# Optimization experiments

Measured on AMD Instinct MI355X. Metric: run time of the kernel, lower is better.

## Reference

```python
import jax, jax.numpy as jnp
import numpy as np

STATE_DIM = 128
NUM_STATES = 16
BATCH = 16384


def setup_inputs() -> dict:
    key = jax.random.key(0)
    k1, k2, k3, k4 = jax.random.split(key, 4)
    x = jax.random.normal(k1, (BATCH, STATE_DIM), dtype=jnp.float32)
    state_idx = jax.random.randint(k2, (BATCH,), 0, NUM_STATES)
    A_all = jax.random.normal(k3, (NUM_STATES, STATE_DIM, STATE_DIM), dtype=jnp.float32)
    C_all = jax.random.normal(k4, (NUM_STATES, STATE_DIM, STATE_DIM), dtype=jnp.float32)
    return {"x": x, "state_idx": state_idx, "A_all": A_all, "C_all": C_all}


def reference(x, state_idx, A_all, C_all):
    # Per-sample expert matrix gather: [B, D, D]
    Ag = A_all[state_idx]
    Cg = C_all[state_idx]
    # state = relu(x @ A_i) per sample, batched via einsum
    state = jax.nn.relu(jnp.einsum('bd,bde->be', x, Ag))
    # observation = state @ C_i
    out = jnp.einsum('be,bef->bf', state, Cg)
    return out
```

## Files before the change

kernel.cpp:

```cpp
#include <hip/hip_runtime.h>

#define D 128
#define NS 16
#define BATCH 16384
#define TILE 32
#define NTB 32

typedef __attribute__((ext_vector_type(8))) short short8;
typedef __attribute__((ext_vector_type(4))) float f32x4;

__device__ __forceinline__ unsigned short f2bf(float f) {
  unsigned u = __builtin_bit_cast(unsigned, f);
  u += 0x7FFFu + ((u >> 16) & 1u);
  return (unsigned short)(u >> 16);
}

#define CPAD 32

__global__ __launch_bounds__(256) void prep_kernel(
    const float* __restrict__ A_all, const float* __restrict__ C_all,
    const int* __restrict__ sidx,
    int* __restrict__ counts, unsigned short* __restrict__ lists,
    unsigned short* __restrict__ At, unsigned short* __restrict__ Ct) {
  const int b = blockIdx.x, tid = threadIdx.x;
  if (b < 128) {
    __shared__ float T[32][129];
    const int mat = b >> 6, r = b & 63, s = r >> 2, slab = r & 3;
    const float* in = (mat ? C_all : A_all) + (size_t)s * D * D;
    unsigned short* outp = (mat ? Ct : At) + (size_t)s * D * D;
    const int e0 = slab * 32;
    const int ecol = (tid & 7) * 4;
    const int drow = tid >> 3;
#pragma unroll
    for (int i = 0; i < 4; i++) {
      const int d = drow + 32 * i;
      const float4 v = *(const float4*)(in + (size_t)d * D + e0 + ecol);
      T[ecol + 0][d] = v.x;
      T[ecol + 1][d] = v.y;
      T[ecol + 2][d] = v.z;
      T[ecol + 3][d] = v.w;
    }
    __syncthreads();
    const int e = tid >> 3;
    const int d0 = (tid & 7) * 16;
    unsigned short p[16];
#pragma unroll
    for (int k = 0; k < 16; k++) p[k] = f2bf(T[e][d0 + k]);
    unsigned short* dst = outp + (size_t)(e0 + e) * D + d0;
    *(uint4*)(dst) = *(const uint4*)(p);
    *(uint4*)(dst + 8) = *(const uint4*)(p + 8);
  } else {
    __shared__ int wcnt[4][NS];
    __shared__ int woff[4][NS];
    __shared__ int sbase[NS];
    const int i = (b - 128) * 256 + tid;
    const int s = sidx[i];
    const int lane = tid & 63, w = tid >> 6;
    int myrank = 0;
#pragma unroll 1
    for (int ss = 0; ss < NS; ss++) {
      unsigned long long m = __ballot(s == ss);
      if (s == ss) myrank = (int)__popcll(m & ((1ull << lane) - 1ull));
      if (lane == 0) wcnt[w][ss] = (int)__popcll(m);
    }
    __syncthreads();
    if (tid < NS) {
      const int c0 = wcnt[0][tid], c1 = wcnt[1][tid];
      const int c2 = wcnt[2][tid], c3 = wcnt[3][tid];
      sbase[tid] = atomicAdd(&counts[tid * CPAD], c0 + c1 + c2 + c3);
      woff[0][tid] = 0;
      woff[1][tid] = c0;
      woff[2][tid] = c0 + c1;
      woff[3][tid] = c0 + c1 + c2;
    }
    __syncthreads();
    lists[(size_t)s * BATCH + sbase[s] + woff[w][s] + myrank] = (unsigned short)i;
  }
}

__global__ __launch_bounds__(256, 3) void ssm_kernel(
    const float* __restrict__ x,
    const int* __restrict__ counts,
    const unsigned short* __restrict__ lists,
    const unsigned short* __restrict__ At,
    const unsigned short* __restrict__ Ct,
    float* __restrict__ out) {
  __shared__ unsigned short Xs[TILE][136];
  __shared__ unsigned short Hs[TILE][136];
  __shared__ unsigned short Ws[D][136];
  __shared__ int rows[TILE];

  const int s = blockIdx.y;
  const int n = counts[s * CPAD];
  const int tid = threadIdx.x;
  const int lane = tid & 63, w = tid >> 6;
  const int l15 = lane & 15, quad = lane >> 4;
  const int wr = w & 1, wc = w >> 1;

  for (int t0 = blockIdx.x; t0 * TILE < n; t0 += NTB) {
    if (t0 != blockIdx.x) __syncthreads();
    const int row0 = t0 * TILE;
    const int nr = min(TILE, n - row0);
    const size_t lb = (size_t)s * BATCH + row0;

    uint4 ctr[8];
    {
      const uint4* g = (const uint4*)(Ct + (size_t)s * D * D);
#pragma unroll
      for (int i = 0; i < 8; i++) ctr[i] = g[i * 256 + tid];
    }

    {
      const int r = tid >> 3, q = tid & 7;
      int rid = (r < nr) ? (int)lists[lb + r] : -1;
      if (q == 0) rows[r] = rid;
      unsigned short* xr = &Xs[r][q * 16];
      if (rid >= 0) {
        const float4* src = (const float4*)(x + (size_t)rid * D + q * 16);
#pragma unroll
        for (int i = 0; i < 4; i++) {
          float4 v = src[i];
          ushort4 p;
          p.x = f2bf(v.x); p.y = f2bf(v.y); p.z = f2bf(v.z); p.w = f2bf(v.w);
          *(ushort4*)(xr + i * 4) = p;
        }
      } else {
        ushort4 z; z.x = z.y = z.z = z.w = 0;
#pragma unroll
        for (int i = 0; i < 4; i++) *(ushort4*)(xr + i * 4) = z;
      }
    }
    {
      const uint4* g = (const uint4*)(At + (size_t)s * D * D);
#pragma unroll
      for (int i = 0; i < 8; i++) {
        const int c = i * 256 + tid;
        *(uint4*)&Ws[c >> 4][(c & 15) * 8] = g[c];
      }
    }
    __syncthreads();

    f32x4 acc[4];
#pragma unroll
    for (int nb = 0; nb < 4; nb++) acc[nb] = (f32x4){0.f, 0.f, 0.f, 0.f};
#pragma unroll
    for (int kb = 0; kb < 4; kb++) {
      short8 aF = *(const short8*)&Xs[wr * 16 + l15][kb * 32 + quad * 8];
#pragma unroll
      for (int nb = 0; nb < 4; nb++) {
        short8 bF = *(const short8*)&Ws[wc * 64 + nb * 16 + l15][kb * 32 + quad * 8];
        acc[nb] = __builtin_amdgcn_mfma_f32_16x16x32_bf16(aF, bF, acc[nb], 0, 0, 0);
      }
    }
#pragma unroll
    for (int nb = 0; nb < 4; nb++)
#pragma unroll
      for (int r = 0; r < 4; r++) {
        float v = acc[nb][r];
        Hs[wr * 16 + quad * 4 + r][wc * 64 + nb * 16 + l15] = f2bf(v > 0.f ? v : 0.f);
      }
    __syncthreads();

#pragma unroll
    for (int i = 0; i < 8; i++) {
      const int c = i * 256 + tid;
      *(uint4*)&Ws[c >> 4][(c & 15) * 8] = ctr[i];
    }
    __syncthreads();

#pragma unroll
    for (int nb = 0; nb < 4; nb++) acc[nb] = (f32x4){0.f, 0.f, 0.f, 0.f};
#pragma unroll
    for (int kb = 0; kb < 4; kb++) {
      short8 aF = *(const short8*)&Hs[wr * 16 + l15][kb * 32 + quad * 8];
#pragma unroll
      for (int nb = 0; nb < 4; nb++) {
        short8 bF = *(const short8*)&Ws[wc * 64 + nb * 16 + l15][kb * 32 + quad * 8];
        acc[nb] = __builtin_amdgcn_mfma_f32_16x16x32_bf16(aF, bF, acc[nb], 0, 0, 0);
      }
    }

#pragma unroll
    for (int r = 0; r < 4; r++) {
      const int rl = wr * 16 + quad * 4 + r;
      if (rl < nr) {
        float* orow = out + (size_t)rows[rl] * D + wc * 64 + l15;
#pragma unroll
        for (int nb = 0; nb < 4; nb++) orow[nb * 16] = acc[nb][r];
      }
    }
  }
}

extern "C" void kernel_launch(void* const* d_in, const int* in_sizes, int n_in,
                              void* d_out, int out_size, void* d_ws, size_t ws_size,
                              hipStream_t stream) {
  const float* x = (const float*)d_in[0];
  const int* sidx = (const int*)d_in[1];
  const float* A_all = (const float*)d_in[2];
  const float* C_all = (const float*)d_in[3];
  float* out = (float*)d_out;

  int* counts = (int*)d_ws;
  unsigned short* lists = (unsigned short*)((char*)d_ws + 2048);
  unsigned short* At = (unsigned short*)((char*)d_ws + 2048 + 512 * 1024);
  unsigned short* Ct = At + NS * D * D;

  hipMemsetAsync(counts, 0, 2048, stream);
  prep_kernel<<<192, 256, 0, stream>>>(A_all, C_all, sidx, counts, lists, At, Ct);
  ssm_kernel<<<dim3(NTB, NS), 256, 0, stream>>>(x, counts, lists, At, Ct, out);
}
```

Measured before the change: 84.22 us.

## Replace global bucket lists with per-block chunk scan of state indices

Drops the global sorting/bucketing step (memset, atomic counts, index lists) and instead has each (chunk, state) block scan a 512-sample slice of state_idx with ballots, building a local row list in shared memory. Both A and C bf16 matrices are now held in registers for the whole block, so they are loaded from global memory only once per block. Occupancy hint drops from 3 to 2 blocks per CU. Each block now covers about 32 rows, so tiles are often partly filled, and the index array is read once for each of the 16 states.

```diff
diff --git a/kernel.cpp b/kernel.cpp
--- a/kernel.cpp
+++ b/kernel.cpp
@@ -4,7 +4,8 @@
 #define NS 16
 #define BATCH 16384
 #define TILE 32
-#define NTB 32
+#define CHUNK 512
+#define NCH (BATCH / CHUNK)
 
 typedef __attribute__((ext_vector_type(8))) short short8;
 typedef __attribute__((ext_vector_type(4))) float f32x4;
@@ -15,105 +16,94 @@
   return (unsigned short)(u >> 16);
 }
 
-#define CPAD 32
-
 __global__ __launch_bounds__(256) void prep_kernel(
     const float* __restrict__ A_all, const float* __restrict__ C_all,
-    const int* __restrict__ sidx,
-    int* __restrict__ counts, unsigned short* __restrict__ lists,
     unsigned short* __restrict__ At, unsigned short* __restrict__ Ct) {
   const int b = blockIdx.x, tid = threadIdx.x;
-  if (b < 128) {
-    __shared__ float T[32][129];
-    const int mat = b >> 6, r = b & 63, s = r >> 2, slab = r & 3;
-    const float* in = (mat ? C_all : A_all) + (size_t)s * D * D;
-    unsigned short* outp = (mat ? Ct : At) + (size_t)s * D * D;
-    const int e0 = slab * 32;
-    const int ecol = (tid & 7) * 4;
-    const int drow = tid >> 3;
+  __shared__ float T[32][129];
+  const int mat = b >> 6, r = b & 63, s = r >> 2, slab = r & 3;
+  const float* in = (mat ? C_all : A_all) + (size_t)s * D * D;
+  unsigned short* outp = (mat ? Ct : At) + (size_t)s * D * D;
+  const int e0 = slab * 32;
+  const int ecol = (tid & 7) * 4;
+  const int drow = tid >> 3;
 #pragma unroll
-    for (int i = 0; i < 4; i++) {
-      const int d = drow + 32 * i;
-      const float4 v = *(const float4*)(in + (size_t)d * D + e0 + ecol);
-      T[ecol + 0][d] = v.x;
-      T[ecol + 1][d] = v.y;
-      T[ecol + 2][d] = v.z;
-      T[ecol + 3][d] = v.w;
-    }
-    __syncthreads();
-    const int e = tid >> 3;
-    const int d0 = (tid & 7) * 16;
-    unsigned short p[16];
+  for (int i = 0; i < 4; i++) {
+    const int d = drow + 32 * i;
+    const float4 v = *(const float4*)(in + (size_t)d * D + e0 + ecol);
+    T[ecol + 0][d] = v.x;
+    T[ecol + 1][d] = v.y;
+    T[ecol + 2][d] = v.z;
+    T[ecol + 3][d] = v.w;
+  }
+  __syncthreads();
+  const int e = tid >> 3;
+  const int d0 = (tid & 7) * 16;
+  unsigned short p[16];
 #pragma unroll
-    for (int k = 0; k < 16; k++) p[k] = f2bf(T[e][d0 + k]);
-    unsigned short* dst = outp + (size_t)(e0 + e) * D + d0;
-    *(uint4*)(dst) = *(const uint4*)(p);
-    *(uint4*)(dst + 8) = *(const uint4*)(p + 8);
-  } else {
-    __shared__ int wcnt[4][NS];
-    __shared__ int woff[4][NS];
-    __shared__ int sbase[NS];
-    const int i = (b - 128) * 256 + tid;
-    const int s = sidx[i];
-    const int lane = tid & 63, w = tid >> 6;
-    int myrank = 0;
-#pragma unroll 1
-    for (int ss = 0; ss < NS; ss++) {
-      unsigned long long m = __ballot(s == ss);
-      if (s == ss) myrank = (int)__popcll(m & ((1ull << lane) - 1ull));
-      if (lane == 0) wcnt[w][ss] = (int)__popcll(m);
-    }
-    __syncthreads();
-    if (tid < NS) {
-      const int c0 = wcnt[0][tid], c1 = wcnt[1][tid];
-      const int c2 = wcnt[2][tid], c3 = wcnt[3][tid];
-      sbase[tid] = atomicAdd(&counts[tid * CPAD], c0 + c1 + c2 + c3);
-      woff[0][tid] = 0;
-      woff[1][tid] = c0;
-      woff[2][tid] = c0 + c1;
-      woff[3][tid] = c0 + c1 + c2;
-    }
-    __syncthreads();
-    lists[(size_t)s * BATCH + sbase[s] + woff[w][s] + myrank] = (unsigned short)i;
-  }
+  for (int k = 0; k < 16; k++) p[k] = f2bf(T[e][d0 + k]);
+  unsigned short* dst = outp + (size_t)(e0 + e) * D + d0;
+  *(uint4*)(dst) = *(const uint4*)(p);
+  *(uint4*)(dst + 8) = *(const uint4*)(p + 8);
 }
 
-__global__ __launch_bounds__(256, 3) void ssm_kernel(
+__global__ __launch_bounds__(256, 2) void ssm_kernel(
     const float* __restrict__ x,
-    const int* __restrict__ counts,
-    const unsigned short* __restrict__ lists,
+    const int* __restrict__ sidx,
     const unsigned short* __restrict__ At,
     const unsigned short* __restrict__ Ct,
     float* __restrict__ out) {
   __shared__ unsigned short Xs[TILE][136];
   __shared__ unsigned short Hs[TILE][136];
   __shared__ unsigned short Ws[D][136];
-  __shared__ int rows[TILE];
+  __shared__ int rowlist[CHUNK];
+  __shared__ int wcnt[8];
 
   const int s = blockIdx.y;
-  const int n = counts[s * CPAD];
+  const int c0 = blockIdx.x * CHUNK;
   const int tid = threadIdx.x;
   const int lane = tid & 63, w = tid >> 6;
   const int l15 = lane & 15, quad = lane >> 4;
   const int wr = w & 1, wc = w >> 1;
 
-  for (int t0 = blockIdx.x; t0 * TILE < n; t0 += NTB) {
-    if (t0 != blockIdx.x) __syncthreads();
-    const int row0 = t0 * TILE;
-    const int nr = min(TILE, n - row0);
-    const size_t lb = (size_t)s * BATCH + row0;
+  uint4 atr[8], ctr[8];
+  {
+    const uint4* gA = (const uint4*)(At + (size_t)s * D * D);
+    const uint4* gC = (const uint4*)(Ct + (size_t)s * D * D);
+#pragma unroll
+    for (int i = 0; i < 8; i++) { atr[i] = gA[i * 256 + tid]; ctr[i] = gC[i * 256 + tid]; }
+  }
 
-    uint4 ctr[8];
-    {
-      const uint4* g = (const uint4*)(Ct + (size_t)s * D * D);
+  const int v0 = sidx[c0 + tid];
+  const int v1 = sidx[c0 + 256 + tid];
+  const unsigned long long lanelt = (1ull << lane) - 1ull;
+  const unsigned long long m0 = __ballot(v0 == s);
+  const unsigned long long m1 = __ballot(v1 == s);
+  if (lane == 0) { wcnt[w] = (int)__popcll(m0); wcnt[4 + w] = (int)__popcll(m1); }
+  __syncthreads();
+  int pre0 = 0, pre1 = 0, tot0 = 0, cnt = 0;
 #pragma unroll
-      for (int i = 0; i < 8; i++) ctr[i] = g[i * 256 + tid];
+  for (int ww = 0; ww < 4; ww++) {
+    if (ww < w) { pre0 += wcnt[ww]; pre1 += wcnt[4 + ww]; }
+    tot0 += wcnt[ww];
+    cnt += wcnt[ww] + wcnt[4 + ww];
+  }
+  if (v0 == s) rowlist[pre0 + (int)__popcll(m0 & lanelt)] = c0 + tid;
+  if (v1 == s) rowlist[tot0 + pre1 + (int)__popcll(m1 & lanelt)] = c0 + 256 + tid;
+  __syncthreads();
+
+  for (int i0 = 0; i0 < cnt; i0 += TILE) {
+    if (i0) __syncthreads();
+
+#pragma unroll
+    for (int i = 0; i < 8; i++) {
+      const int c = i * 256 + tid;
+      *(uint4*)&Ws[c >> 4][(c & 15) * 8] = atr[i];
     }
-
     {
       const int r = tid >> 3, q = tid & 7;
-      int rid = (r < nr) ? (int)lists[lb + r] : -1;
-      if (q == 0) rows[r] = rid;
+      const int rl = i0 + r;
+      const int rid = (rl < cnt) ? rowlist[rl] : -1;
       unsigned short* xr = &Xs[r][q * 16];
       if (rid >= 0) {
         const float4* src = (const float4*)(x + (size_t)rid * D + q * 16);
@@ -128,14 +118,6 @@
         ushort4 z; z.x = z.y = z.z = z.w = 0;
 #pragma unroll
         for (int i = 0; i < 4; i++) *(ushort4*)(xr + i * 4) = z;
-      }
-    }
-    {
-      const uint4* g = (const uint4*)(At + (size_t)s * D * D);
-#pragma unroll
-      for (int i = 0; i < 8; i++) {
-        const int c = i * 256 + tid;
-        *(uint4*)&Ws[c >> 4][(c & 15) * 8] = g[c];
       }
     }
     __syncthreads();
@@ -155,9 +137,9 @@
 #pragma unroll
     for (int nb = 0; nb < 4; nb++)
 #pragma unroll
-      for (int r = 0; r < 4; r++) {
-        float v = acc[nb][r];
-        Hs[wr * 16 + quad * 4 + r][wc * 64 + nb * 16 + l15] = f2bf(v > 0.f ? v : 0.f);
+      for (int rr = 0; rr < 4; rr++) {
+        float v = acc[nb][rr];
+        Hs[wr * 16 + quad * 4 + rr][wc * 64 + nb * 16 + l15] = f2bf(v > 0.f ? v : 0.f);
       }
     __syncthreads();
 
@@ -181,12 +163,12 @@
     }
 
 #pragma unroll
-    for (int r = 0; r < 4; r++) {
-      const int rl = wr * 16 + quad * 4 + r;
-      if (rl < nr) {
-        float* orow = out + (size_t)rows[rl] * D + wc * 64 + l15;
+    for (int rr = 0; rr < 4; rr++) {
+      const int rl = wr * 16 + quad * 4 + rr;
+      if (i0 + rl < cnt) {
+        float* orow = out + (size_t)rowlist[i0 + rl] * D + wc * 64 + l15;
 #pragma unroll
-        for (int nb = 0; nb < 4; nb++) orow[nb * 16] = acc[nb][r];
+        for (int nb = 0; nb < 4; nb++) orow[nb * 16] = acc[nb][rr];
       }
     }
   }
@@ -201,12 +183,9 @@
   const float* C_all = (const float*)d_in[3];
   float* out = (float*)d_out;
 
-  int* counts = (int*)d_ws;
-  unsigned short* lists = (unsigned short*)((char*)d_ws + 2048);
-  unsigned short* At = (unsigned short*)((char*)d_ws + 2048 + 512 * 1024);
+  unsigned short* At = (unsigned short*)d_ws;
   unsigned short* Ct = At + NS * D * D;
 
-  hipMemsetAsync(counts, 0, 2048, stream);
-  prep_kernel<<<192, 256, 0, stream>>>(A_all, C_all, sidx, counts, lists, At, Ct);
-  ssm_kernel<<<dim3(NTB, NS), 256, 0, stream>>>(x, counts, lists, At, Ct, out);
+  prep_kernel<<<128, 256, 0, stream>>>(A_all, C_all, At, Ct);
+  ssm_kernel<<<dim3(NCH, NS), 256, 0, stream>>>(x, sidx, At, Ct, out);
 }
```

After: 88.40 us. 5.0% more time.
